# Optimization experiments

Hardware: AMD Instinct MI355X
Metric: run time of the kernel (lower is better)

The kernel has to match this reference:

```python
import jax, jax.numpy as jnp
import numpy as np

SIZE = (96, 160, 160)  # (D, H, W) from init_kwargs


def grid_sample_3d(inp, grid, padding_mode):
    """PyTorch-semantics 3D grid_sample, trilinear, align_corners=True.
    inp: (B, C, D, H, W); grid: (B, Do, Ho, Wo, 3) with grid[...,0]=x(W), [...,1]=y(H), [...,2]=z(D).
    """
    B, C, D, H, W = inp.shape
    x = (grid[..., 0] + 1.0) * 0.5 * (W - 1)
    y = (grid[..., 1] + 1.0) * 0.5 * (H - 1)
    z = (grid[..., 2] + 1.0) * 0.5 * (D - 1)
    if padding_mode == 'border':
        x = jnp.clip(x, 0.0, W - 1)
        y = jnp.clip(y, 0.0, H - 1)
        z = jnp.clip(z, 0.0, D - 1)
    x0f, y0f, z0f = jnp.floor(x), jnp.floor(y), jnp.floor(z)
    fx, fy, fz = x - x0f, y - y0f, z - z0f
    x0, y0, z0 = x0f.astype(jnp.int32), y0f.astype(jnp.int32), z0f.astype(jnp.int32)
    x1, y1, z1 = x0 + 1, y0 + 1, z0 + 1

    flat = inp.reshape(B, C, D * H * W)
    Do, Ho, Wo = grid.shape[1:4]
    N = Do * Ho * Wo

    def corner(zi, yi, xi, w):
        if padding_mode == 'zeros':
            valid = ((zi >= 0) & (zi < D) & (yi >= 0) & (yi < H) & (xi >= 0) & (xi < W))
            w = w * valid.astype(inp.dtype)
        zi = jnp.clip(zi, 0, D - 1)
        yi = jnp.clip(yi, 0, H - 1)
        xi = jnp.clip(xi, 0, W - 1)
        idx = ((zi * H + yi) * W + xi).reshape(B, 1, N)
        vals = jnp.take_along_axis(flat, idx, axis=2).reshape(B, C, Do, Ho, Wo)
        return vals * w[:, None]

    out = (corner(z0, y0, x0, (1 - fz) * (1 - fy) * (1 - fx))
           + corner(z0, y0, x1, (1 - fz) * (1 - fy) * fx)
           + corner(z0, y1, x0, (1 - fz) * fy * (1 - fx))
           + corner(z0, y1, x1, (1 - fz) * fy * fx)
           + corner(z1, y0, x0, fz * (1 - fy) * (1 - fx))
           + corner(z1, y0, x1, fz * (1 - fy) * fx)
           + corner(z1, y1, x0, fz * fy * (1 - fx))
           + corner(z1, y1, x1, fz * fy * fx))
    return out


def make_grid():
    D, H, W = SIZE
    g = jnp.stack(jnp.meshgrid(jnp.arange(D), jnp.arange(H), jnp.arange(W), indexing='ij'))
    return g[None].astype(jnp.float32)  # (1, 3, D, H, W)


def setup_inputs() -> dict:
    key = jax.random.key(0)
    k1, k2 = jax.random.split(key)
    D, H, W = SIZE
    src = jax.random.normal(k1, (1, 1, D, H, W), dtype=jnp.float32)
    flows = jax.random.normal(k2, (3, 1, 3, D, H, W), dtype=jnp.float32)
    range_flow = jnp.float32(0.4)
    return {"src": src, "flows": flows, "range_flow": range_flow}


def reference(src, flows, range_flow):
    D, H, W = SIZE
    grid = make_grid()  # (1, 3, D, H, W)
    shape = jnp.array([D, H, W], dtype=jnp.float32).reshape(-1, 1, 1, 1)
    acc = jnp.zeros_like(grid)
    for i in range(flows.shape[0]):  # small fixed number of flow stages
        flow = flows[i]
        ng = 2.0 * (grid / shape) - 1.0
        warped = grid_sample_3d(flow, jnp.transpose(ng, (0, 2, 3, 4, 1)), 'border')
        acc = acc + warped
    final = grid + acc * range_flow
    denom = jnp.array([D - 1, H - 1, W - 1], dtype=jnp.float32).reshape(-1, 1, 1, 1)
    final = 2.0 * (final / denom - 0.5)
    fg = jnp.transpose(final, (0, 2, 3, 4, 1))
    return grid_sample_3d(src, fg, 'zeros')
```

## Files before the change

kernel.cpp:

```cpp
#include <hip/hip_runtime.h>
#include <stdint.h>

constexpr int Dz = 96, Hy = 160, Wx = 160;
constexpr int NVOX = Dz * Hy * Wx;

constexpr int ZW = 6, YW = 2, XP = 56;
constexpr int ROWS = ZW * YW;
constexpr int NCHUNK = ROWS * 14;
constexpr int UI = 3;
constexpr int WBUF = UI * 64 * 4;

#define WAIT_LGKM() do { asm volatile("s_waitcnt lgkmcnt(0)" ::: "memory"); \
                         __builtin_amdgcn_sched_barrier(0); } while (0)
#define FENCE() __builtin_amdgcn_sched_barrier(0)

__global__ __launch_bounds__(128) void st_fused_kernel(
    const float* __restrict__ src,
    const float* __restrict__ flows,
    const float* __restrict__ rfp,
    float* __restrict__ out)
{
    __shared__ float raw[2][WBUF];
    const int t = threadIdx.x;
    const int lane = t & 63;

    const int bid = blockIdx.x;
    const int swz = (bid & 7) * 600 + (bid >> 3);
    const int wid = __builtin_amdgcn_readfirstlane(swz * 2 + (t >> 6));
    const int wt = wid % 20;
    const int rest = wid / 20;
    const int dt = rest % 3;
    const int h0 = rest / 3;
    const int w0w = wt * 8, d0 = dt * 32;
    const int v = t >> 6;
    const float rf = *rfp;

    const int Z0w = (19 * w0w) >> 5;
    const int X0 = 53 * dt;
    const int X0a = X0 & ~3;
    const int YB = (159 * h0) / 160;

    const char* ap[UI];
    {
        const char* fb = (const char*)flows + ((size_t)YB * Wx + X0a) * 4;
#pragma unroll
        for (int u = 0; u < UI; ++u) {
            int c = u * 64 + lane;
            if (c >= NCHUNK) c = NCHUNK - 1;
            int row = c / 14, ch = c - row * 14;
            int zr = row >> 1, yr = row & 1;
            ap[u] = fb + ((size_t)(zr * Hy + yr) * Wx + (size_t)Z0w * Hy * Wx) * 4 + ch * 16;
        }
    }

    float* const lb = &raw[v][0];
    float4 bA[3], bB[3];
#define LOADB(SET, U) do { \
    _Pragma("unroll") \
    for (int i = 0; i < 3; ++i) \
        SET[i] = *(const float4*)(ap[U] + (size_t)i * (3u * NVOX * 4u)); \
    ap[U] += (size_t)NVOX * 4; } while (0)
#define STOREB(SET, U) do { \
    float4 s; \
    s.x = (SET[0].x + SET[1].x) + SET[2].x; \
    s.y = (SET[0].y + SET[1].y) + SET[2].y; \
    s.z = (SET[0].z + SET[1].z) + SET[2].z; \
    s.w = (SET[0].w + SET[1].w) + SET[2].w; \
    ((float4*)lb)[(U) * 64 + lane] = s; } while (0)

    const int dl = lane & 31;
    const int half = lane >> 5;
    const int d = d0 + dl;

    const float xf = (float)(53 * d) * (1.0f / 32.0f);
    const int   x0i = (int)xf;
    const float fx  = xf - (float)x0i;
    const int   xx  = x0i - X0a;
    const float wxa = 1.0f - fx, wxb = fx;

    int rowoff[4];
    float wkz[4][4];
    {
        int zzk[4]; float wz0k[4], wz1k[4];
#pragma unroll
        for (int k = 0; k < 4; ++k) {
            const int w = w0w + 4 * half + k;
            const float zf = (float)(19 * w) * (1.0f / 32.0f);
            const int z0i = (int)zf;
            const float fz = zf - (float)z0i;
            zzk[k] = z0i - Z0w;
            wz0k[k] = 1.0f - fz; wz1k[k] = fz;
        }
        const int zz0 = zzk[0];
#pragma unroll
        for (int r = 0; r < 4; ++r) {
            rowoff[r] = min(zz0 + r, ZW - 1) * (YW * XP);
#pragma unroll
            for (int k = 0; k < 4; ++k) {
                const int rel = zzk[k] - zz0;
                wkz[r][k] = (rel == r) ? wz0k[k] : ((rel == r - 1) ? wz1k[k] : 0.0f);
            }
        }
    }

    const float fy = (float)h0 * (159.0f / 160.0f) - (float)YB;
    const float wy0 = 1.0f - fy, wy1 = fy;

    auto compute = [&](float (&acc)[4]) {
#pragma unroll
        for (int yy = 0; yy < 2; ++yy) {
            float zv0 = 0.f, zv1 = 0.f, zv2 = 0.f, zv3 = 0.f;
#pragma unroll
            for (int r = 0; r < 4; ++r) {
                const float* p = lb + rowoff[r] + yy * XP + xx;
                const float xv = wxa * p[0] + wxb * p[1];
                zv0 += wkz[r][0] * xv;
                zv1 += wkz[r][1] * xv;
                zv2 += wkz[r][2] * xv;
                zv3 += wkz[r][3] * xv;
            }
            const float wy = yy ? wy1 : wy0;
            acc[0] += wy * zv0;
            acc[1] += wy * zv1;
            acc[2] += wy * zv2;
            acc[3] += wy * zv3;
        }
    };

    float accA[4] = {0.f, 0.f, 0.f, 0.f};
    float accB[4] = {0.f, 0.f, 0.f, 0.f};
    float accC[4] = {0.f, 0.f, 0.f, 0.f};

    LOADB(bA, 0); LOADB(bB, 1);
    STOREB(bA, 0); LOADB(bA, 2);
    STOREB(bB, 1); STOREB(bA, 2);
    LOADB(bA, 0); LOADB(bB, 1);
    compute(accA);
    FENCE();
    STOREB(bA, 0); LOADB(bA, 2);
    STOREB(bB, 1); STOREB(bA, 2);
    LOADB(bA, 0); LOADB(bB, 1);
    compute(accB);
    FENCE();
    STOREB(bA, 0); LOADB(bA, 2);
    STOREB(bB, 1); STOREB(bA, 2);
    compute(accC);
#undef LOADB
#undef STOREB

    float* tr = &raw[v][0];
#pragma unroll
    for (int k = 0; k < 4; ++k) {
        const int w = w0w + 4 * half + k;
        const float f0 = (float)d + accA[k] * rf;
        const float f1 = (float)h0 + accB[k] * rf;
        const float f2 = (float)w + accC[k] * rf;

        const float xs = f0 * (159.0f / 95.0f);
        const float ys = f1;
        const float zs = f2 * (95.0f / 159.0f);

        const float xf0 = floorf(xs), yf0 = floorf(ys), zf0 = floorf(zs);
        const float gx = xs - xf0, gy = ys - yf0, gz = zs - zf0;
        const int xi0 = (int)xf0, yi0 = (int)yf0, zi0 = (int)zf0;

        const int xc = min(max(xi0, 0), Wx - 2);
        const bool sx0 = (xi0 == xc);
        const float wx0m = ((unsigned)xi0 < (unsigned)Wx) ? (1.0f - gx) : 0.0f;
        const float wx1m = ((unsigned)(xi0 + 1) < (unsigned)Wx) ? gx : 0.0f;

        const int yc0 = min(max(yi0, 0), Hy - 1);
        const int yc1 = min(max(yi0 + 1, 0), Hy - 1);
        const int zc0 = min(max(zi0, 0), Dz - 1);
        const int zc1 = min(max(zi0 + 1, 0), Dz - 1);
        const float wy0m = ((unsigned)yi0 < (unsigned)Hy) ? (1.0f - gy) : 0.0f;
        const float wy1m = ((unsigned)(yi0 + 1) < (unsigned)Hy) ? gy : 0.0f;
        const float wz0m = ((unsigned)zi0 < (unsigned)Dz) ? (1.0f - gz) : 0.0f;
        const float wz1m = ((unsigned)(zi0 + 1) < (unsigned)Dz) ? gz : 0.0f;

        const float w00 = wz0m * wy0m, w01 = wz0m * wy1m;
        const float w10 = wz1m * wy0m, w11 = wz1m * wy1m;

        float r = 0.0f;
        auto rowadd = [&](int zc, int yc, float wt) {
            const float* p = src + ((size_t)zc * Hy + yc) * Wx + xc;
            const float va = p[0], vb = p[1];
            const float s0 = sx0 ? va : vb;
            const float s1 = sx0 ? vb : va;
            r += wt * (wx0m * s0 + wx1m * s1);
        };
        rowadd(zc0, yc0, w00);
        rowadd(zc0, yc1, w01);
        rowadd(zc1, yc0, w10);
        rowadd(zc1, yc1, w11);

        tr[dl * 9 + 4 * half + k] = r;
    }
    WAIT_LGKM();

    const int rrow = lane >> 3;
    const int rcol = lane & 7;
#pragma unroll
    for (int m = 0; m < 4; ++m) {
        const int dr = m * 8 + rrow;
        out[((size_t)(d0 + dr) * Hy + h0) * Wx + (w0w + rcol)] =
            tr[dr * 9 + rcol];
    }
}

extern "C" void kernel_launch(void* const* d_in, const int* in_sizes, int n_in,
                              void* d_out, int out_size, void* d_ws, size_t ws_size,
                              hipStream_t stream) {
    const float* src   = (const float*)d_in[0];
    const float* flows = (const float*)d_in[1];
    const float* rfp   = (const float*)d_in[2];
    float* out = (float*)d_out;

    st_fused_kernel<<<dim3(4800), 128, 0, stream>>>(src, flows, rfp, out);
}
```

Before: 30.63 us.

## Replace LDS-staged flow tile with direct per-lane global float2 loads

Drops the cooperative float4 staging of the flow neighbourhood into shared memory, along with its software-pipelined load/sum/store schedule. Each lane now issues its own float2 global loads for every z-row, y-row, flow stage and component, and sums the three stages in registers before trilinear interpolation. This removes the LDS writes, the LDS reads and the staging bookkeeping. In exchange, many overlapping loads across neighbouring lanes now depend on L1/L2 to serve the reuse, with less coalescing and no explicit overlap between loading and computing.

```diff
diff --git a/kernel.cpp b/kernel.cpp
--- a/kernel.cpp
+++ b/kernel.cpp
@@ -4,15 +4,8 @@
 constexpr int Dz = 96, Hy = 160, Wx = 160;
 constexpr int NVOX = Dz * Hy * Wx;
 
-constexpr int ZW = 6, YW = 2, XP = 56;
-constexpr int ROWS = ZW * YW;
-constexpr int NCHUNK = ROWS * 14;
-constexpr int UI = 3;
-constexpr int WBUF = UI * 64 * 4;
-
 #define WAIT_LGKM() do { asm volatile("s_waitcnt lgkmcnt(0)" ::: "memory"); \
                          __builtin_amdgcn_sched_barrier(0); } while (0)
-#define FENCE() __builtin_amdgcn_sched_barrier(0)
 
 __global__ __launch_bounds__(128) void st_fused_kernel(
     const float* __restrict__ src,
@@ -20,53 +13,22 @@
     const float* __restrict__ rfp,
     float* __restrict__ out)
 {
-    __shared__ float raw[2][WBUF];
+    __shared__ float trbuf[2][292];
     const int t = threadIdx.x;
     const int lane = t & 63;
+    const int v = t >> 6;
 
     const int bid = blockIdx.x;
     const int swz = (bid & 7) * 600 + (bid >> 3);
-    const int wid = __builtin_amdgcn_readfirstlane(swz * 2 + (t >> 6));
+    const int wid = __builtin_amdgcn_readfirstlane(swz * 2 + v);
     const int wt = wid % 20;
     const int rest = wid / 20;
     const int dt = rest % 3;
     const int h0 = rest / 3;
     const int w0w = wt * 8, d0 = dt * 32;
-    const int v = t >> 6;
     const float rf = *rfp;
 
-    const int Z0w = (19 * w0w) >> 5;
-    const int X0 = 53 * dt;
-    const int X0a = X0 & ~3;
     const int YB = (159 * h0) / 160;
-
-    const char* ap[UI];
-    {
-        const char* fb = (const char*)flows + ((size_t)YB * Wx + X0a) * 4;
-#pragma unroll
-        for (int u = 0; u < UI; ++u) {
-            int c = u * 64 + lane;
-            if (c >= NCHUNK) c = NCHUNK - 1;
-            int row = c / 14, ch = c - row * 14;
-            int zr = row >> 1, yr = row & 1;
-            ap[u] = fb + ((size_t)(zr * Hy + yr) * Wx + (size_t)Z0w * Hy * Wx) * 4 + ch * 16;
-        }
-    }
-
-    float* const lb = &raw[v][0];
-    float4 bA[3], bB[3];
-#define LOADB(SET, U) do { \
-    _Pragma("unroll") \
-    for (int i = 0; i < 3; ++i) \
-        SET[i] = *(const float4*)(ap[U] + (size_t)i * (3u * NVOX * 4u)); \
-    ap[U] += (size_t)NVOX * 4; } while (0)
-#define STOREB(SET, U) do { \
-    float4 s; \
-    s.x = (SET[0].x + SET[1].x) + SET[2].x; \
-    s.y = (SET[0].y + SET[1].y) + SET[2].y; \
-    s.z = (SET[0].z + SET[1].z) + SET[2].z; \
-    s.w = (SET[0].w + SET[1].w) + SET[2].w; \
-    ((float4*)lb)[(U) * 64 + lane] = s; } while (0)
 
     const int dl = lane & 31;
     const int half = lane >> 5;
@@ -75,86 +37,83 @@
     const float xf = (float)(53 * d) * (1.0f / 32.0f);
     const int   x0i = (int)xf;
     const float fx  = xf - (float)x0i;
-    const int   xx  = x0i - X0a;
     const float wxa = 1.0f - fx, wxb = fx;
 
-    int rowoff[4];
+    int z0a;
     float wkz[4][4];
     {
-        int zzk[4]; float wz0k[4], wz1k[4];
+        int z0k[4]; float wz0k[4], wz1k[4];
 #pragma unroll
         for (int k = 0; k < 4; ++k) {
             const int w = w0w + 4 * half + k;
             const float zf = (float)(19 * w) * (1.0f / 32.0f);
-            const int z0i = (int)zf;
-            const float fz = zf - (float)z0i;
-            zzk[k] = z0i - Z0w;
-            wz0k[k] = 1.0f - fz; wz1k[k] = fz;
+            const int zi = (int)zf;
+            const float fz = zf - (float)zi;
+            z0k[k] = zi; wz0k[k] = 1.0f - fz; wz1k[k] = fz;
         }
-        const int zz0 = zzk[0];
+        z0a = z0k[0];
 #pragma unroll
-        for (int r = 0; r < 4; ++r) {
-            rowoff[r] = min(zz0 + r, ZW - 1) * (YW * XP);
+        for (int r = 0; r < 4; ++r)
 #pragma unroll
             for (int k = 0; k < 4; ++k) {
-                const int rel = zzk[k] - zz0;
+                const int rel = z0k[k] - z0a;
                 wkz[r][k] = (rel == r) ? wz0k[k] : ((rel == r - 1) ? wz1k[k] : 0.0f);
             }
-        }
     }
 
     const float fy = (float)h0 * (159.0f / 160.0f) - (float)YB;
     const float wy0 = 1.0f - fy, wy1 = fy;
 
-    auto compute = [&](float (&acc)[4]) {
+    const float* rp[4][2];
+#pragma unroll
+    for (int r = 0; r < 4; ++r)
+#pragma unroll
+        for (int yy = 0; yy < 2; ++yy)
+            rp[r][yy] = flows + ((size_t)((z0a + r) * Hy + (YB + yy)) * Wx + x0i);
+
+    float acc[3][4];
+#pragma unroll
+    for (int c = 0; c < 3; ++c)
+#pragma unroll
+        for (int k = 0; k < 4; ++k) acc[c][k] = 0.f;
+
+#pragma unroll
+    for (int c = 0; c < 3; ++c) {
 #pragma unroll
         for (int yy = 0; yy < 2; ++yy) {
+            float2 L[3][4];
+#pragma unroll
+            for (int s = 0; s < 3; ++s)
+#pragma unroll
+                for (int r = 0; r < 4; ++r)
+                    L[s][r] = *(const float2*)(rp[r][yy] + (size_t)(s * 3 + c) * NVOX);
+
             float zv0 = 0.f, zv1 = 0.f, zv2 = 0.f, zv3 = 0.f;
 #pragma unroll
             for (int r = 0; r < 4; ++r) {
-                const float* p = lb + rowoff[r] + yy * XP + xx;
-                const float xv = wxa * p[0] + wxb * p[1];
+                const float p0 = (L[0][r].x + L[1][r].x) + L[2][r].x;
+                const float p1 = (L[0][r].y + L[1][r].y) + L[2][r].y;
+                const float xv = wxa * p0 + wxb * p1;
                 zv0 += wkz[r][0] * xv;
                 zv1 += wkz[r][1] * xv;
                 zv2 += wkz[r][2] * xv;
                 zv3 += wkz[r][3] * xv;
             }
             const float wy = yy ? wy1 : wy0;
-            acc[0] += wy * zv0;
-            acc[1] += wy * zv1;
-            acc[2] += wy * zv2;
-            acc[3] += wy * zv3;
+            acc[c][0] += wy * zv0;
+            acc[c][1] += wy * zv1;
+            acc[c][2] += wy * zv2;
+            acc[c][3] += wy * zv3;
         }
-    };
+    }
 
-    float accA[4] = {0.f, 0.f, 0.f, 0.f};
-    float accB[4] = {0.f, 0.f, 0.f, 0.f};
-    float accC[4] = {0.f, 0.f, 0.f, 0.f};
-
-    LOADB(bA, 0); LOADB(bB, 1);
-    STOREB(bA, 0); LOADB(bA, 2);
-    STOREB(bB, 1); STOREB(bA, 2);
-    LOADB(bA, 0); LOADB(bB, 1);
-    compute(accA);
-    FENCE();
-    STOREB(bA, 0); LOADB(bA, 2);
-    STOREB(bB, 1); STOREB(bA, 2);
-    LOADB(bA, 0); LOADB(bB, 1);
-    compute(accB);
-    FENCE();
-    STOREB(bA, 0); LOADB(bA, 2);
-    STOREB(bB, 1); STOREB(bA, 2);
-    compute(accC);
-#undef LOADB
-#undef STOREB
-
-    float* tr = &raw[v][0];
+    float* tr = &trbuf[v][0];
 #pragma unroll
     for (int k = 0; k < 4; ++k) {
         const int w = w0w + 4 * half + k;
-        const float f0 = (float)d + accA[k] * rf;
-        const float f1 = (float)h0 + accB[k] * rf;
-        const float f2 = (float)w + accC[k] * rf;
+        const float f0 = (float)d + acc[0][k] * rf;
+        const float f1 = (float)h0 + acc[1][k] * rf;
+        const float f2 = (float)w + acc[2][k] * rf;
 
         const float xs = f0 * (159.0f / 95.0f);
         const float ys = f1;
```

New measurement: 36.75 us. 1.2x slower.

## Share flow-sum LDS tile across four h-rows per 256-thread block

Applied to the files above, without the earlier changes.

Each block now has four waves, one per output h row, and they cooperatively load a single 6x5-row flow tile into shared memory instead of each wave loading its own 6x2-row tile. This cuts redundant global loads of overlapping y rows between neighbouring h rows. Double-buffered LDS stages for the three flow channels are handed over with __syncthreads. The exchange is block-wide barriers and larger shared memory use, which may lower occupancy.

```diff
diff --git a/kernel.cpp b/kernel.cpp
--- a/kernel.cpp
+++ b/kernel.cpp
@@ -4,35 +4,35 @@
 constexpr int Dz = 96, Hy = 160, Wx = 160;
 constexpr int NVOX = Dz * Hy * Wx;
 
-constexpr int ZW = 6, YW = 2, XP = 56;
+constexpr int ZW = 6, YW = 5, XP = 56;
 constexpr int ROWS = ZW * YW;
 constexpr int NCHUNK = ROWS * 14;
-constexpr int UI = 3;
-constexpr int WBUF = UI * 64 * 4;
+constexpr int PL = ROWS * XP;
 
 #define WAIT_LGKM() do { asm volatile("s_waitcnt lgkmcnt(0)" ::: "memory"); \
                          __builtin_amdgcn_sched_barrier(0); } while (0)
 #define FENCE() __builtin_amdgcn_sched_barrier(0)
 
-__global__ __launch_bounds__(128) void st_fused_kernel(
+__global__ __launch_bounds__(256) void st_fused_kernel(
     const float* __restrict__ src,
     const float* __restrict__ flows,
     const float* __restrict__ rfp,
     float* __restrict__ out)
 {
-    __shared__ float raw[2][WBUF];
+    __shared__ float bufA[PL], bufB[PL];
+    __shared__ float trb[4][292];
     const int t = threadIdx.x;
     const int lane = t & 63;
+    const int v = t >> 6;
 
     const int bid = blockIdx.x;
-    const int swz = (bid & 7) * 600 + (bid >> 3);
-    const int wid = __builtin_amdgcn_readfirstlane(swz * 2 + (t >> 6));
-    const int wt = wid % 20;
-    const int rest = wid / 20;
+    const int swz = (bid & 7) * 300 + (bid >> 3);
+    const int wt = swz % 20;
+    const int rest = swz / 20;
     const int dt = rest % 3;
-    const int h0 = rest / 3;
-    const int w0w = wt * 8, d0 = dt * 32;
-    const int v = t >> 6;
+    const int hq = rest / 3;
+    const int w0w = wt * 8, d0 = dt * 32, h0 = hq * 4;
+    const int h = h0 + v;
     const float rf = *rfp;
 
     const int Z0w = (19 * w0w) >> 5;
@@ -40,33 +40,43 @@
     const int X0a = X0 & ~3;
     const int YB = (159 * h0) / 160;
 
-    const char* ap[UI];
+    const char* ap[2];
+    int loff[2];
     {
         const char* fb = (const char*)flows + ((size_t)YB * Wx + X0a) * 4;
 #pragma unroll
-        for (int u = 0; u < UI; ++u) {
-            int c = u * 64 + lane;
+        for (int u = 0; u < 2; ++u) {
+            int c = t + u * 256;
             if (c >= NCHUNK) c = NCHUNK - 1;
             int row = c / 14, ch = c - row * 14;
-            int zr = row >> 1, yr = row & 1;
-            ap[u] = fb + ((size_t)(zr * Hy + yr) * Wx + (size_t)Z0w * Hy * Wx) * 4 + ch * 16;
-        }
-    }
-
-    float* const lb = &raw[v][0];
-    float4 bA[3], bB[3];
-#define LOADB(SET, U) do { \
-    _Pragma("unroll") \
-    for (int i = 0; i < 3; ++i) \
-        SET[i] = *(const float4*)(ap[U] + (size_t)i * (3u * NVOX * 4u)); \
-    ap[U] += (size_t)NVOX * 4; } while (0)
-#define STOREB(SET, U) do { \
-    float4 s; \
-    s.x = (SET[0].x + SET[1].x) + SET[2].x; \
-    s.y = (SET[0].y + SET[1].y) + SET[2].y; \
-    s.z = (SET[0].z + SET[1].z) + SET[2].z; \
-    s.w = (SET[0].w + SET[1].w) + SET[2].w; \
-    ((float4*)lb)[(U) * 64 + lane] = s; } while (0)
+            int zr = row / YW, yr = row - zr * YW;
+            ap[u] = fb + ((size_t)((Z0w + zr) * Hy + yr) * Wx) * 4 + ch * 16;
+            loff[u] = row * XP + ch * 4;
+        }
+    }
+
+    float4 rg[2][3];
+    auto issue_ch = [&]() {
+#pragma unroll
+        for (int u = 0; u < 2; ++u) {
+            rg[u][0] = *(const float4*)(ap[u]);
+            rg[u][1] = *(const float4*)(ap[u] + (size_t)3 * NVOX * 4);
+            rg[u][2] = *(const float4*)(ap[u] + (size_t)6 * NVOX * 4);
+        }
+#pragma unroll
+        for (int u = 0; u < 2; ++u) ap[u] += (size_t)NVOX * 4;
+    };
+    auto commit_ch = [&](float* dst) {
+#pragma unroll
+        for (int u = 0; u < 2; ++u) {
+            float4 s;
+            s.x = (rg[u][0].x + rg[u][1].x) + rg[u][2].x;
+            s.y = (rg[u][0].y + rg[u][1].y) + rg[u][2].y;
+            s.z = (rg[u][0].z + rg[u][1].z) + rg[u][2].z;
+            s.w = (rg[u][0].w + rg[u][1].w) + rg[u][2].w;
+            *(float4*)(dst + loff[u]) = s;
+        }
+    };
 
     const int dl = lane & 31;
     const int half = lane >> 5;
@@ -103,23 +113,26 @@
         }
     }
 
-    const float fy = (float)h0 * (159.0f / 160.0f) - (float)YB;
+    const float yf = (float)h * (159.0f / 160.0f);
+    const int y0i = (int)yf;
+    const float fy = yf - (float)y0i;
+    const int yrel = y0i - YB;
     const float wy0 = 1.0f - fy, wy1 = fy;
 
-    auto compute = [&](float (&acc)[4]) {
+    auto compute = [&](const float* buf, float (&acc)[4]) {
 #pragma unroll
         for (int yy = 0; yy < 2; ++yy) {
+            const float wy = yy ? wy1 : wy0;
             float zv0 = 0.f, zv1 = 0.f, zv2 = 0.f, zv3 = 0.f;
 #pragma unroll
             for (int r = 0; r < 4; ++r) {
-                const float* p = lb + rowoff[r] + yy * XP + xx;
+                const float* p = buf + rowoff[r] + (yrel + yy) * XP + xx;
                 const float xv = wxa * p[0] + wxb * p[1];
                 zv0 += wkz[r][0] * xv;
                 zv1 += wkz[r][1] * xv;
                 zv2 += wkz[r][2] * xv;
                 zv3 += wkz[r][3] * xv;
             }
-            const float wy = yy ? wy1 : wy0;
             acc[0] += wy * zv0;
             acc[1] += wy * zv1;
             acc[2] += wy * zv2;
@@ -131,29 +144,27 @@
     float accB[4] = {0.f, 0.f, 0.f, 0.f};
     float accC[4] = {0.f, 0.f, 0.f, 0.f};
 
-    LOADB(bA, 0); LOADB(bB, 1);
-    STOREB(bA, 0); LOADB(bA, 2);
-    STOREB(bB, 1); STOREB(bA, 2);
-    LOADB(bA, 0); LOADB(bB, 1);
-    compute(accA);
+    issue_ch();
+    commit_ch(bufA);
+    __syncthreads();
+    issue_ch();
+    compute(bufA, accA);
     FENCE();
-    STOREB(bA, 0); LOADB(bA, 2);
-    STOREB(bB, 1); STOREB(bA, 2);
-    LOADB(bA, 0); LOADB(bB, 1);
-    compute(accB);
+    commit_ch(bufB);
+    __syncthreads();
+    issue_ch();
+    compute(bufB, accB);
     FENCE();
-    STOREB(bA, 0); LOADB(bA, 2);
-    STOREB(bB, 1); STOREB(bA, 2);
-    compute(accC);
-#undef LOADB
-#undef STOREB
-
-    float* tr = &raw[v][0];
+    commit_ch(bufA);
+    __syncthreads();
+    compute(bufA, accC);
+
+    float* tr = &trb[v][0];
 #pragma unroll
     for (int k = 0; k < 4; ++k) {
         const int w = w0w + 4 * half + k;
         const float f0 = (float)d + accA[k] * rf;
-        const float f1 = (float)h0 + accB[k] * rf;
+        const float f1 = (float)h + accB[k] * rf;
         const float f2 = (float)w + accC[k] * rf;
 
         const float xs = f0 * (159.0f / 95.0f);
@@ -182,12 +193,12 @@
         const float w10 = wz1m * wy0m, w11 = wz1m * wy1m;
 
         float r = 0.0f;
-        auto rowadd = [&](int zc, int yc, float wt) {
+        auto rowadd = [&](int zc, int yc, float wgt) {
             const float* p = src + ((size_t)zc * Hy + yc) * Wx + xc;
             const float va = p[0], vb = p[1];
             const float s0 = sx0 ? va : vb;
             const float s1 = sx0 ? vb : va;
-            r += wt * (wx0m * s0 + wx1m * s1);
+            r += wgt * (wx0m * s0 + wx1m * s1);
         };
         rowadd(zc0, yc0, w00);
         rowadd(zc0, yc1, w01);
@@ -203,7 +214,7 @@
 #pragma unroll
     for (int m = 0; m < 4; ++m) {
         const int dr = m * 8 + rrow;
-        out[((size_t)(d0 + dr) * Hy + h0) * Wx + (w0w + rcol)] =
+        out[((size_t)(d0 + dr) * Hy + h) * Wx + (w0w + rcol)] =
             tr[dr * 9 + rcol];
     }
 }
@@ -216,5 +227,5 @@
     const float* rfp   = (const float*)d_in[2];
     float* out = (float*)d_out;
 
-    st_fused_kernel<<<dim3(4800), 128, 0, stream>>>(src, flows, rfp, out);
+    st_fused_kernel<<<dim3(2400), 256, 0, stream>>>(src, flows, rfp, out);
 }
```

Result: faster. 29.06 us (median of 2 runs) (-5.1%).
